# Kernel optimization log

Measured on AMD Instinct MI355X. Metric: run time of the kernel, lower is better.

Reference implementation:

```python
import jax, jax.numpy as jnp
import numpy as np

DIM = 1024
NUM_HEADS = 16
HEAD_DIM = DIM // NUM_HEADS


def setup_inputs() -> dict:
    key = jax.random.key(0)
    ks = jax.random.split(key, 5)
    x = jax.random.normal(ks[0], (2, 4096, DIM), dtype=jnp.float32)
    # nn.Linear(dim, 3*dim): weight [3D, D], bias [3D]; we store transposed [D, 3D]
    scale = 1.0 / np.sqrt(DIM)
    w_qkv = jax.random.normal(ks[1], (DIM, 3 * DIM), dtype=jnp.float32) * scale
    b_qkv = jax.random.normal(ks[2], (3 * DIM,), dtype=jnp.float32) * scale
    w_o = jax.random.normal(ks[3], (DIM, DIM), dtype=jnp.float32) * scale
    b_o = jax.random.normal(ks[4], (DIM,), dtype=jnp.float32) * scale
    return {"x": x, "w_qkv": w_qkv, "b_qkv": b_qkv, "w_o": w_o, "b_o": b_o}


def reference(x, w_qkv, b_qkv, w_o, b_o):
    b, n, _ = x.shape
    h, d = NUM_HEADS, HEAD_DIM
    qkv = x @ w_qkv + b_qkv                      # [B, N, 3D]
    q, k, v = jnp.split(qkv, 3, axis=-1)
    # [B, N, H, d] -> [B, H, N, d]
    q = q.reshape(b, n, h, d).transpose(0, 2, 1, 3)
    k = k.reshape(b, n, h, d).transpose(0, 2, 1, 3)
    v = v.reshape(b, n, h, d).transpose(0, 2, 1, 3)
    scale = 1.0 / np.sqrt(d).astype(np.float32)
    score = jnp.einsum("bhqd,bhkd->bhqk", q, k) * scale   # [B, H, N, N]
    attn = jax.nn.softmax(score, axis=-1)
    out = jnp.einsum("bhqk,bhkd->bhqd", attn, v)          # [B, H, N, d]
    out = out.transpose(0, 2, 1, 3).reshape(b, n, h * d)  # [B, N, D]
    return out @ w_o + b_o
```

## Files before the change

### kernel.cpp

```cpp
#include <hip/hip_runtime.h>

typedef __attribute__((ext_vector_type(8))) __bf16 bf16x8;
typedef __attribute__((ext_vector_type(8))) short short8;
typedef __attribute__((ext_vector_type(4))) float f32x4;

__device__ __forceinline__ unsigned short f2bf(float f) {
    union { float f; unsigned int i; } c; c.f = f;
    unsigned int r = c.i + 0x7fffu + ((c.i >> 16) & 1u);
    return (unsigned short)(r >> 16);
}

__device__ __forceinline__ unsigned int cvt_pk_bf16(float lo, float hi) {
    unsigned int r;
    asm("v_cvt_pk_bf16_f32 %0, %1, %2" : "=v"(r) : "v"(lo), "v"(hi));
    return r;
}

#if __has_builtin(__builtin_amdgcn_exp2f)
#define FAST_EXP2(x) __builtin_amdgcn_exp2f(x)
#else
#define FAST_EXP2(x) __expf((x) * 0.6931471805599453f)
#endif

__device__ __forceinline__ void async_cp16(const unsigned short* g, unsigned short* l) {
    __builtin_amdgcn_global_load_lds(
        (const __attribute__((address_space(1))) unsigned int*)g,
        (__attribute__((address_space(3))) unsigned int*)l, 16, 0, 0);
}

#define DIM 1024
#define NSEQ 4096
#define NH 16
#define HD 64

#define SWZ(row, col) (((row) << 6) + ((col) ^ (((row) & 7) << 3)))

__global__ __launch_bounds__(256)
void conv_kernel(const float* __restrict__ in, unsigned short* __restrict__ out)
{
    const int i = blockIdx.x * 256 + threadIdx.x;
    const float4 a0 = ((const float4*)in)[i * 2];
    const float4 a1 = ((const float4*)in)[i * 2 + 1];
    short8 v;
    v[0] = (short)f2bf(a0.x); v[1] = (short)f2bf(a0.y);
    v[2] = (short)f2bf(a0.z); v[3] = (short)f2bf(a0.w);
    v[4] = (short)f2bf(a1.x); v[5] = (short)f2bf(a1.y);
    v[6] = (short)f2bf(a1.z); v[7] = (short)f2bf(a1.w);
    ((short8*)out)[i] = v;
}

template<int N, int K>
__global__ __launch_bounds__(256)
void transpose_conv_kernel(const float* __restrict__ in, unsigned short* __restrict__ out)
{
    __shared__ unsigned short Ls[64][65];
    const int t  = threadIdx.x;
    const int k0 = blockIdx.x * 64, n0 = blockIdx.y * 64;
    const int kl = t >> 2, nl = (t & 3) * 16;
    const float* src = in + (size_t)(k0 + kl) * N + n0 + nl;
    #pragma unroll
    for (int i = 0; i < 4; i++) {
        float4 a = *(const float4*)(src + i * 4);
        Ls[kl][nl + i*4 + 0] = f2bf(a.x); Ls[kl][nl + i*4 + 1] = f2bf(a.y);
        Ls[kl][nl + i*4 + 2] = f2bf(a.z); Ls[kl][nl + i*4 + 3] = f2bf(a.w);
    }
    __syncthreads();
    const int kl2 = (t & 7) * 8;
    #pragma unroll
    for (int i = 0; i < 2; i++) {
        const int nl2 = (t >> 3) + i * 32;
        short8 v;
        #pragma unroll
        for (int j = 0; j < 8; j++) v[j] = (short)Ls[kl2 + j][nl2];
        *(short8*)(out + (size_t)(n0 + nl2) * K + k0 + kl2) = v;
    }
}

template<int MODE>
__global__ __launch_bounds__(256)
void gemm_kernel(const unsigned short* __restrict__ A,
                 const unsigned short* __restrict__ Bt,
                 const float* __restrict__ bias,
                 unsigned short* __restrict__ out0,
                 unsigned short* __restrict__ out1,
                 unsigned short* __restrict__ out2,
                 float* __restrict__ outf)
{
    __shared__ __align__(16) unsigned short As[128][32];
    __shared__ __align__(16) unsigned short Bs[128][32];
    const int t    = threadIdx.x;
    const int m0   = blockIdx.x * 128, n0 = blockIdx.y * 128;
    const int lane = t & 63, wv = t >> 6;
    const int l15  = lane & 15, quad = lane >> 4;
    const int wm   = (wv >> 1) * 64, wn = (wv & 1) * 64;
    const int sr   = wv * 16 + (lane >> 2);
    const int sc   = (lane & 3) * 8;
    const unsigned short* Ag = A  + (size_t)m0 * 1024;
    const unsigned short* Bg = Bt + (size_t)n0 * 1024;

    f32x4 acc[4][4] = {};

    for (int kt = 0; kt < 1024; kt += 32) {
        __syncthreads();
        async_cp16(Ag + (size_t)(sr)      * 1024 + kt + sc, &As[sr][sc]);
        async_cp16(Ag + (size_t)(sr + 64) * 1024 + kt + sc, &As[sr + 64][sc]);
        async_cp16(Bg + (size_t)(sr)      * 1024 + kt + sc, &Bs[sr][sc]);
        async_cp16(Bg + (size_t)(sr + 64) * 1024 + kt + sc, &Bs[sr + 64][sc]);
        __syncthreads();

        bf16x8 af[4], bfr[4];
        #pragma unroll
        for (int mi = 0; mi < 4; mi++) af[mi]  = *(const bf16x8*)&As[wm + mi*16 + l15][quad*8];
        #pragma unroll
        for (int ni = 0; ni < 4; ni++) bfr[ni] = *(const bf16x8*)&Bs[wn + ni*16 + l15][quad*8];
        #pragma unroll
        for (int mi = 0; mi < 4; mi++)
            #pragma unroll
            for (int ni = 0; ni < 4; ni++)
                acc[mi][ni] = __builtin_amdgcn_mfma_f32_16x16x32_bf16(af[mi], bfr[ni], acc[mi][ni], 0, 0, 0);
    }

    #pragma unroll
    for (int mi = 0; mi < 4; mi++) {
        #pragma unroll
        for (int ni = 0; ni < 4; ni++) {
            const int col  = n0 + wn + ni*16 + l15;
            const float bval = bias[col];
            #pragma unroll
            for (int r = 0; r < 4; r++) {
                const int row = m0 + wm + mi*16 + quad*4 + r;
                const float val = acc[mi][ni][r] + bval;
                if (MODE == 0) {
                    const int which = col >> 10;
                    const int rem   = col & 1023;
                    const int h = rem >> 6, dd = rem & 63;
                    const int bb = row >> 12, ns = row & 4095;
                    if (which == 2) {
                        out2[((size_t)((bb * NH + h) * HD + dd)) * NSEQ + ns] = f2bf(val);
                    } else {
                        const size_t off = ((size_t)((bb * NH + h) * NSEQ + ns)) * HD + dd;
                        ((which == 0) ? out0 : out1)[off] = f2bf(val);
                    }
                } else {
                    outf[(size_t)row * 1024 + col] = val;
                }
            }
        }
    }
}

#define C_LOG2E 0.1803368801111183f
#define M_LOG2  11.541560327111707f

__global__ __launch_bounds__(256, 4)
void attn_kernel(const unsigned short* __restrict__ qb,
                 const unsigned short* __restrict__ kb,
                 const unsigned short* __restrict__ vb,
                 unsigned short* __restrict__ ob)
{
    __shared__ __align__(16) unsigned short Ks[64 * 64];
    __shared__ __align__(16) unsigned short Vt[64 * 64];
    __shared__ __align__(16) unsigned short Ps[4][32 * 64];

    const int t    = threadIdx.x;
    const int wv   = t >> 6, lane = t & 63, l15 = lane & 15, quad = lane >> 4;
    const int q0   = blockIdx.x * 128;
    const int h    = blockIdx.y, b = blockIdx.z;
    const size_t bh = (size_t)(b * NH + h) * NSEQ * HD;
    const unsigned short* Qp  = qb + bh;
    const unsigned short* Kp  = kb + bh;
    const unsigned short* Vtp = vb + bh;

    bf16x8 aq[2][2];
    #pragma unroll
    for (int mi = 0; mi < 2; mi++) {
        const unsigned short* qrow =
            Qp + (size_t)(q0 + wv*32 + mi*16 + l15) * HD + quad*8;
        aq[mi][0] = *(const bf16x8*)(qrow);
        aq[mi][1] = *(const bf16x8*)(qrow + 32);
    }

    float l_loc[2] = {};
    f32x4 acc_o[2][4] = {};

    const int sr = t >> 2, sc = (t & 3) * 16;
    const int ks0 = SWZ(sr, sc), ks1 = SWZ(sr, sc + 8);

    short8 kv0 = *(const short8*)(Kp  + (size_t)sr * HD + sc);
    short8 kv1 = *(const short8*)(Kp  + (size_t)sr * HD + sc + 8);
    short8 vv0 = *(const short8*)(Vtp + (size_t)sr * NSEQ + sc);
    short8 vv1 = *(const short8*)(Vtp + (size_t)sr * NSEQ + sc + 8);

    for (int kt = 0; kt < NSEQ; kt += 64) {
        __syncthreads();
        *(short8*)&Ks[ks0] = kv0;
        *(short8*)&Ks[ks1] = kv1;
        *(short8*)&Vt[ks0] = vv0;
        *(short8*)&Vt[ks1] = vv1;
        __syncthreads();

        const int ktn = (kt + 64) & (NSEQ - 1);
        kv0 = *(const short8*)(Kp  + (size_t)(ktn + sr) * HD + sc);
        kv1 = *(const short8*)(Kp  + (size_t)(ktn + sr) * HD + sc + 8);
        vv0 = *(const short8*)(Vtp + (size_t)sr * NSEQ + ktn + sc);
        vv1 = *(const short8*)(Vtp + (size_t)sr * NSEQ + ktn + sc + 8);

        f32x4 accs[2][4] = {};
        __builtin_amdgcn_s_setprio(1);
        #pragma unroll
        for (int nj = 0; nj < 4; nj++) {
            bf16x8 bk0 = *(const bf16x8*)&Ks[SWZ(nj*16 + l15, quad*8)];
            bf16x8 bk1 = *(const bf16x8*)&Ks[SWZ(nj*16 + l15, 32 + quad*8)];
            #pragma unroll
            for (int mi = 0; mi < 2; mi++) {
                accs[mi][nj] = __builtin_amdgcn_mfma_f32_16x16x32_bf16(bk0, aq[mi][0], accs[mi][nj], 0, 0, 0);
                accs[mi][nj] = __builtin_amdgcn_mfma_f32_16x16x32_bf16(bk1, aq[mi][1], accs[mi][nj], 0, 0, 0);
            }
        }
        __builtin_amdgcn_s_setprio(0);

        #pragma unroll
        for (int mi = 0; mi < 2; mi++) {
            #pragma unroll
            for (int nj = 0; nj < 4; nj++) {
                const float p0 = FAST_EXP2(fmaf(accs[mi][nj][0], C_LOG2E, -M_LOG2));
                const float p1 = FAST_EXP2(fmaf(accs[mi][nj][1], C_LOG2E, -M_LOG2));
                const float p2 = FAST_EXP2(fmaf(accs[mi][nj][2], C_LOG2E, -M_LOG2));
                const float p3 = FAST_EXP2(fmaf(accs[mi][nj][3], C_LOG2E, -M_LOG2));
                l_loc[mi] += (p0 + p1) + (p2 + p3);
                uint2 w;
                w.x = cvt_pk_bf16(p0, p1);
                w.y = cvt_pk_bf16(p2, p3);
                *(uint2*)&Ps[wv][SWZ(mi*16 + l15, nj*16 + quad*4)] = w;
            }
        }
        asm volatile("s_waitcnt lgkmcnt(0)" ::: "memory");
        __builtin_amdgcn_sched_barrier(0);

        bf16x8 ap[2][2];
        #pragma unroll
        for (int mi = 0; mi < 2; mi++) {
            ap[mi][0] = *(const bf16x8*)&Ps[wv][SWZ(mi*16 + l15, quad*8)];
            ap[mi][1] = *(const bf16x8*)&Ps[wv][SWZ(mi*16 + l15, 32 + quad*8)];
        }
        __builtin_amdgcn_s_setprio(1);
        #pragma unroll
        for (int nj = 0; nj < 4; nj++) {
            bf16x8 bv0 = *(const bf16x8*)&Vt[SWZ(nj*16 + l15, quad*8)];
            bf16x8 bv1 = *(const bf16x8*)&Vt[SWZ(nj*16 + l15, 32 + quad*8)];
            #pragma unroll
            for (int mi = 0; mi < 2; mi++) {
                acc_o[mi][nj] = __builtin_amdgcn_mfma_f32_16x16x32_bf16(ap[mi][0], bv0, acc_o[mi][nj], 0, 0, 0);
                acc_o[mi][nj] = __builtin_amdgcn_mfma_f32_16x16x32_bf16(ap[mi][1], bv1, acc_o[mi][nj], 0, 0, 0);
            }
        }
        __builtin_amdgcn_s_setprio(0);
    }

    #pragma unroll
    for (int mi = 0; mi < 2; mi++) {
        float l = l_loc[mi];
        l += __shfl_xor(l, 16);
        l += __shfl_xor(l, 32);
        #pragma unroll
        for (int r = 0; r < 4; r++) {
            const float inv = 1.0f / __shfl(l, quad*4 + r, 16);
            const int row = q0 + wv*32 + mi*16 + quad*4 + r;
            const size_t base = ((size_t)(b * NSEQ + row)) * DIM + h * HD;
            #pragma unroll
            for (int nj = 0; nj < 4; nj++)
                ob[base + nj*16 + l15] = f2bf(acc_o[mi][nj][r] * inv);
        }
    }
}

extern "C" void kernel_launch(void* const* d_in, const int* in_sizes, int n_in,
                              void* d_out, int out_size, void* d_ws, size_t ws_size,
                              hipStream_t stream)
{
    const float *x = nullptr, *w_qkv = nullptr, *b_qkv = nullptr,
                *w_o = nullptr, *b_o = nullptr;
    for (int i = 0; i < n_in; i++) {
        switch (in_sizes[i]) {
            case 8388608: x     = (const float*)d_in[i]; break;
            case 3145728: w_qkv = (const float*)d_in[i]; break;
            case 3072:    b_qkv = (const float*)d_in[i]; break;
            case 1048576: w_o   = (const float*)d_in[i]; break;
            case 1024:    b_o   = (const float*)d_in[i]; break;
        }
    }
    float* out = (float*)d_out;

    const size_t WQB  = (size_t)3072 * 1024;
    const size_t WOB  = (size_t)1024 * 1024;
    const size_t SEGB = (size_t)NSEQ * DIM;

    char* p = (char*)d_ws;
    unsigned short* wqb = (unsigned short*)p;  p += WQB * 2;
    unsigned short* wob = (unsigned short*)p;  p += WOB * 2;

    transpose_conv_kernel<3072, 1024><<<dim3(16, 48), 256, 0, stream>>>(w_qkv, wqb);
    transpose_conv_kernel<1024, 1024><<<dim3(16, 16), 256, 0, stream>>>(w_o, wob);

    const size_t tier1_bytes = (WQB + WOB + 2*SEGB + 3*2*SEGB) * 2;
    if (ws_size >= tier1_bytes) {
        unsigned short* xb = (unsigned short*)p;  p += 2 * SEGB * 2;
        unsigned short* qb = (unsigned short*)p;  p += 2 * SEGB * 2;
        unsigned short* kb = (unsigned short*)p;  p += 2 * SEGB * 2;
        unsigned short* vb = (unsigned short*)p;
        unsigned short* ao = xb;
        conv_kernel<<<4096, 256, 0, stream>>>(x, xb);
        gemm_kernel<0><<<dim3(64, 24), 256, 0, stream>>>(xb, wqb, b_qkv, qb, kb, vb, nullptr);
        attn_kernel<<<dim3(32, NH, 2), 256, 0, stream>>>(qb, kb, vb, ao);
        gemm_kernel<1><<<dim3(64, 8), 256, 0, stream>>>(ao, wob, b_o, nullptr, nullptr, nullptr, out);
    } else {
        unsigned short* xb = (unsigned short*)p;  p += SEGB * 2;
        unsigned short* qb = (unsigned short*)p;  p += SEGB * 2;
        unsigned short* kb = (unsigned short*)p;  p += SEGB * 2;
        unsigned short* vb = (unsigned short*)p;
        unsigned short* ao = xb;
        for (int b = 0; b < 2; b++) {
            conv_kernel<<<2048, 256, 0, stream>>>(x + b * SEGB, xb);
            gemm_kernel<0><<<dim3(32, 24), 256, 0, stream>>>(xb, wqb, b_qkv, qb, kb, vb, nullptr);
            attn_kernel<<<dim3(32, NH, 1), 256, 0, stream>>>(qb, kb, vb, ao);
            gemm_kernel<1><<<dim3(32, 8), 256, 0, stream>>>(ao, wob, b_o, nullptr, nullptr, nullptr, out + b * SEGB);
        }
    }
}
```

Measured before the change: 381.0 us.

## Double-buffer K/V with async global-to-LDS loads and keep P in registers

Replaces the register-staged K/V prefetch with `global_load_lds` async copies into two ping-pong LDS buffers. This cuts the loop from two barriers per tile to one and lets the next tile's load overlap compute. It also drops the per-wave P staging buffer in LDS: the bf16 probabilities are packed straight from the QK accumulators into MFMA A operands. To make that work, V^T is read with a permuted key index that matches the accumulator layout. The risks are that the XOR source swizzle must match SWZ, and that correctness depends on the async loads finishing before the barrier.

```diff
diff --git a/kernel.cpp b/kernel.cpp
--- a/kernel.cpp
+++ b/kernel.cpp
@@ -3,6 +3,7 @@
 typedef __attribute__((ext_vector_type(8))) __bf16 bf16x8;
 typedef __attribute__((ext_vector_type(8))) short short8;
 typedef __attribute__((ext_vector_type(4))) float f32x4;
+typedef __attribute__((ext_vector_type(2))) unsigned int uint32x2;
 
 __device__ __forceinline__ unsigned short f2bf(float f) {
     union { float f; unsigned int i; } c; c.f = f;
@@ -14,6 +15,13 @@
     unsigned int r;
     asm("v_cvt_pk_bf16_f32 %0, %1, %2" : "=v"(r) : "v"(lo), "v"(hi));
     return r;
+}
+
+__device__ __forceinline__ bf16x8 pack_bf16x8(unsigned int a, unsigned int b,
+                                              unsigned int c, unsigned int d) {
+    union { unsigned int u[4]; bf16x8 v; } x;
+    x.u[0] = a; x.u[1] = b; x.u[2] = c; x.u[3] = d;
+    return x.v;
 }
 
 #if __has_builtin(__builtin_amdgcn_exp2f)
@@ -158,9 +166,8 @@
                  const unsigned short* __restrict__ vb,
                  unsigned short* __restrict__ ob)
 {
-    __shared__ __align__(16) unsigned short Ks[64 * 64];
-    __shared__ __align__(16) unsigned short Vt[64 * 64];
-    __shared__ __align__(16) unsigned short Ps[4][32 * 64];
+    __shared__ __align__(16) unsigned short Ks[2][64 * 64];
+    __shared__ __align__(16) unsigned short Vt[2][64 * 64];
 
     const int t    = threadIdx.x;
     const int wv   = t >> 6, lane = t & 63, l15 = lane & 15, quad = lane >> 4;
@@ -183,34 +190,45 @@
     float l_loc[2] = {};
     f32x4 acc_o[2][4] = {};
 
-    const int sr = t >> 2, sc = (t & 3) * 16;
-    const int ks0 = SWZ(sr, sc), ks1 = SWZ(sr, sc + 8);
-
-    short8 kv0 = *(const short8*)(Kp  + (size_t)sr * HD + sc);
-    short8 kv1 = *(const short8*)(Kp  + (size_t)sr * HD + sc + 8);
-    short8 vv0 = *(const short8*)(Vtp + (size_t)sr * NSEQ + sc);
-    short8 vv1 = *(const short8*)(Vtp + (size_t)sr * NSEQ + sc + 8);
-
+    const int srow = lane >> 3;
+    const int sg8  = ((lane & 7) ^ srow) * 8;
+    const int rA   = wv * 16 + srow;
+    const int rB   = rA + 8;
+    unsigned short* ldsKA0 = &Ks[0][(wv*16 + 0) * 64];
+    unsigned short* ldsKB0 = &Ks[0][(wv*16 + 8) * 64];
+    unsigned short* ldsVA0 = &Vt[0][(wv*16 + 0) * 64];
+    unsigned short* ldsVB0 = &Vt[0][(wv*16 + 8) * 64];
+    unsigned short* ldsKA1 = &Ks[1][(wv*16 + 0) * 64];
+    unsigned short* ldsKB1 = &Ks[1][(wv*16 + 8) * 64];
+    unsigned short* ldsVA1 = &Vt[1][(wv*16 + 0) * 64];
+    unsigned short* ldsVB1 = &Vt[1][(wv*16 + 8) * 64];
+
+    async_cp16(Kp  + (size_t)rA * HD + sg8,   ldsKA0);
+    async_cp16(Kp  + (size_t)rB * HD + sg8,   ldsKB0);
+    async_cp16(Vtp + (size_t)rA * NSEQ + sg8, ldsVA0);
+    async_cp16(Vtp + (size_t)rB * NSEQ + sg8, ldsVB0);
+
+    int cur = 0;
     for (int kt = 0; kt < NSEQ; kt += 64) {
         __syncthreads();
-        *(short8*)&Ks[ks0] = kv0;
-        *(short8*)&Ks[ks1] = kv1;
-        *(short8*)&Vt[ks0] = vv0;
-        *(short8*)&Vt[ks1] = vv1;
-        __syncthreads();
-
-        const int ktn = (kt + 64) & (NSEQ - 1);
-        kv0 = *(const short8*)(Kp  + (size_t)(ktn + sr) * HD + sc);
-        kv1 = *(const short8*)(Kp  + (size_t)(ktn + sr) * HD + sc + 8);
-        vv0 = *(const short8*)(Vtp + (size_t)sr * NSEQ + ktn + sc);
-        vv1 = *(const short8*)(Vtp + (size_t)sr * NSEQ + ktn + sc + 8);
+
+        if (kt + 64 < NSEQ) {
+            const int ktn = kt + 64;
+            async_cp16(Kp  + (size_t)(ktn + rA) * HD + sg8, cur ? ldsKA0 : ldsKA1);
+            async_cp16(Kp  + (size_t)(ktn + rB) * HD + sg8, cur ? ldsKB0 : ldsKB1);
+            async_cp16(Vtp + (size_t)rA * NSEQ + ktn + sg8, cur ? ldsVA0 : ldsVA1);
+            async_cp16(Vtp + (size_t)rB * NSEQ + ktn + sg8, cur ? ldsVB0 : ldsVB1);
+        }
+
+        const unsigned short* Kc = Ks[cur];
+        const unsigned short* Vc = Vt[cur];
 
         f32x4 accs[2][4] = {};
         __builtin_amdgcn_s_setprio(1);
         #pragma unroll
         for (int nj = 0; nj < 4; nj++) {
-            bf16x8 bk0 = *(const bf16x8*)&Ks[SWZ(nj*16 + l15, quad*8)];
-            bf16x8 bk1 = *(const bf16x8*)&Ks[SWZ(nj*16 + l15, 32 + quad*8)];
+            bf16x8 bk0 = *(const bf16x8*)&Kc[SWZ(nj*16 + l15, quad*8)];
+            bf16x8 bk1 = *(const bf16x8*)&Kc[SWZ(nj*16 + l15, 32 + quad*8)];
             #pragma unroll
             for (int mi = 0; mi < 2; mi++) {
                 accs[mi][nj] = __builtin_amdgcn_mfma_f32_16x16x32_bf16(bk0, aq[mi][0], accs[mi][nj], 0, 0, 0);
@@ -219,6 +237,7 @@
         }
         __builtin_amdgcn_s_setprio(0);
 
+        uint2 pw[2][4];
         #pragma unroll
         for (int mi = 0; mi < 2; mi++) {
             #pragma unroll
@@ -228,33 +247,31 @@
                 const float p2 = FAST_EXP2(fmaf(accs[mi][nj][2], C_LOG2E, -M_LOG2));
                 const float p3 = FAST_EXP2(fmaf(accs[mi][nj][3], C_LOG2E, -M_LOG2));
                 l_loc[mi] += (p0 + p1) + (p2 + p3);
-                uint2 w;
-                w.x = cvt_pk_bf16(p0, p1);
-                w.y = cvt_pk_bf16(p2, p3);
-                *(uint2*)&Ps[wv][SWZ(mi*16 + l15, nj*16 + quad*4)] = w;
+                pw[mi][nj].x = cvt_pk_bf16(p0, p1);
+                pw[mi][nj].y = cvt_pk_bf16(p2, p3);
             }
         }
-        asm volatile("s_waitcnt lgkmcnt(0)" ::: "memory");
-        __builtin_amdgcn_sched_barrier(0);
-
-        bf16x8 ap[2][2];
-        #pragma unroll
-        for (int mi = 0; mi < 2; mi++) {
-            ap[mi][0] = *(const bf16x8*)&Ps[wv][SWZ(mi*16 + l15, quad*8)];
-            ap[mi][1] = *(const bf16x8*)&Ps[wv][SWZ(mi*16 + l15, 32 + quad*8)];
-        }
+
         __builtin_amdgcn_s_setprio(1);
         #pragma unroll
-        for (int nj = 0; nj < 4; nj++) {
-            bf16x8 bv0 = *(const bf16x8*)&Vt[SWZ(nj*16 + l15, quad*8)];
-            bf16x8 bv1 = *(const bf16x8*)&Vt[SWZ(nj*16 + l15, 32 + quad*8)];
-            #pragma unroll
-            for (int mi = 0; mi < 2; mi++) {
-                acc_o[mi][nj] = __builtin_amdgcn_mfma_f32_16x16x32_bf16(ap[mi][0], bv0, acc_o[mi][nj], 0, 0, 0);
-                acc_o[mi][nj] = __builtin_amdgcn_mfma_f32_16x16x32_bf16(ap[mi][1], bv1, acc_o[mi][nj], 0, 0, 0);
+        for (int njd = 0; njd < 4; njd++) {
+            const int drow = njd * 16 + l15;
+            #pragma unroll
+            for (int W = 0; W < 2; W++) {
+                const uint32x2 lo = *(const uint32x2*)&Vc[SWZ(drow, W*32 + quad*4)];
+                const uint32x2 hi = *(const uint32x2*)&Vc[SWZ(drow, W*32 + 16 + quad*4)];
+                const bf16x8 bv = pack_bf16x8(lo[0], lo[1], hi[0], hi[1]);
+                #pragma unroll
+                for (int mi = 0; mi < 2; mi++) {
+                    const bf16x8 ap = pack_bf16x8(pw[mi][2*W].x,   pw[mi][2*W].y,
+                                                  pw[mi][2*W+1].x, pw[mi][2*W+1].y);
+                    acc_o[mi][njd] = __builtin_amdgcn_mfma_f32_16x16x32_bf16(ap, bv, acc_o[mi][njd], 0, 0, 0);
+                }
             }
         }
         __builtin_amdgcn_s_setprio(0);
+
+        cur ^= 1;
     }
 
     #pragma unroll
```

New measurement: 360.9 us (median of 2 runs). -5.3%, faster.
